# Optimization experiments

Measured on AMD Instinct MI355X. Metric: run time of the kernel, lower is better.

The kernel has to match this reference:

```python
import jax, jax.numpy as jnp
import numpy as np

D = 256      # d_model
NH = 8       # heads
HD = D // NH # head dim = 32
NL = 4       # feature levels
NP = 4       # sampling points per head per level
DFF = 1024   # ffn hidden
LAYERS = 6
SHAPES = [(48, 48), (24, 24), (12, 12), (6, 6)]


def setup_inputs() -> dict:
    key = jax.random.key(0)
    ks = jax.random.split(key, 20)
    bs = 2
    inp = {}
    for i, (h, w) in enumerate(SHAPES):
        inp[f"src{i}"] = jax.random.normal(ks[i], (bs, D, h, w), jnp.float32)
        inp[f"pos{i}"] = jax.random.normal(ks[4 + i], (bs, D, h, w), jnp.float32)

    def p(k, shape, s=0.02):
        return jax.random.normal(k, shape, jnp.float32) * s

    inp["level_embed"] = p(ks[8], (NL, D), 1.0)
    inp["Wv"] = p(ks[9], (LAYERS, D, D))
    inp["bv"] = jnp.zeros((LAYERS, D))
    inp["Woff"] = p(ks[10], (LAYERS, D, NH * NL * NP * 2), 0.001)
    inp["boff"] = p(ks[11], (LAYERS, NH * NL * NP * 2), 0.5)
    inp["Wa"] = p(ks[12], (LAYERS, D, NH * NL * NP))
    inp["ba"] = jnp.zeros((LAYERS, NH * NL * NP))
    inp["Wo"] = p(ks[13], (LAYERS, D, D))
    inp["bo"] = jnp.zeros((LAYERS, D))
    inp["g1"] = jnp.ones((LAYERS, D))
    inp["beta1"] = jnp.zeros((LAYERS, D))
    inp["W1"] = p(ks[14], (LAYERS, D, DFF))
    inp["bf1"] = jnp.zeros((LAYERS, DFF))
    inp["W2"] = p(ks[15], (LAYERS, DFF, D))
    inp["bf2"] = jnp.zeros((LAYERS, D))
    inp["g2"] = jnp.ones((LAYERS, D))
    inp["beta2"] = jnp.zeros((LAYERS, D))
    return inp


def _ln(x, g, b):
    m = x.mean(-1, keepdims=True)
    v = ((x - m) ** 2).mean(-1, keepdims=True)
    return (x - m) / jnp.sqrt(v + 1e-5) * g + b


def _bilinear(value, loc, H, W):
    # value: (bs, NH, H*W, HD); loc: (bs, Len, NH, NP, 2) in [0,1]
    # grid_sample, align_corners=False, zero padding
    bs, Len, nh, P, _ = loc.shape
    x = loc[..., 0] * W - 0.5
    y = loc[..., 1] * H - 0.5
    x0 = jnp.floor(x)
    y0 = jnp.floor(y)
    lx = x - x0
    ly = y - y0
    x0i = x0.astype(jnp.int32)
    y0i = y0.astype(jnp.int32)
    out = jnp.zeros((bs, nh, Len, P, value.shape[-1]), value.dtype)
    for dy, dx, w in ((0, 0, (1 - lx) * (1 - ly)), (0, 1, lx * (1 - ly)),
                      (1, 0, (1 - lx) * ly), (1, 1, lx * ly)):
        xi = x0i + dx
        yi = y0i + dy
        valid = (xi >= 0) & (xi < W) & (yi >= 0) & (yi < H)
        idx = jnp.clip(yi, 0, H - 1) * W + jnp.clip(xi, 0, W - 1)  # (bs,Len,NH,P)
        idx_t = idx.transpose(0, 2, 1, 3).reshape(bs, nh, Len * P)
        v = jnp.take_along_axis(value, idx_t[..., None], axis=2)
        v = v.reshape(bs, nh, Len, P, -1)
        wm = (w * valid).transpose(0, 2, 1, 3)  # (bs,NH,Len,P)
        out = out + v * wm[..., None]
    return out


def _msda(q, src, ref, shapes, starts, Wv, bv, Woff, boff, Wa, ba, Wo, bo):
    bs, Len, _ = q.shape
    value = (src @ Wv + bv).reshape(bs, Len, NH, HD)
    off = (q @ Woff + boff).reshape(bs, Len, NH, NL, NP, 2)
    attn = jax.nn.softmax((q @ Wa + ba).reshape(bs, Len, NH, NL * NP), -1)
    attn = attn.reshape(bs, Len, NH, NL, NP)
    acc = jnp.zeros((bs, NH, Len, HD), q.dtype)
    for lv, (H, W) in enumerate(shapes):
        norm = jnp.array([W, H], q.dtype)
        loc = ref[None, :, None, None, :] + off[:, :, :, lv] / norm  # (bs,Len,NH,NP,2)
        v = value[:, starts[lv]:starts[lv] + H * W].transpose(0, 2, 1, 3)
        samp = _bilinear(v, loc, H, W)  # (bs,NH,Len,NP,HD)
        acc = acc + (samp * attn[:, :, :, lv].transpose(0, 2, 1, 3)[..., None]).sum(3)
    return acc.transpose(0, 2, 1, 3).reshape(bs, Len, D) @ Wo + bo


def _encode(srcs, poss, level_embed, Wv, bv, Woff, boff, Wa, ba, Wo, bo,
            g1, beta1, W1, bf1, W2, bf2, g2, beta2):
    shapes = [(s.shape[2], s.shape[3]) for s in srcs]
    bs = srcs[0].shape[0]
    src_flat = jnp.concatenate(
        [s.reshape(bs, D, -1).transpose(0, 2, 1) for s in srcs], 1)
    pos_flat = jnp.concatenate(
        [p.reshape(bs, D, -1).transpose(0, 2, 1) + level_embed[i][None, None]
         for i, p in enumerate(poss)], 1)
    starts = np.cumsum([0] + [h * w for h, w in shapes])[:-1]
    # reference points (masks are all-zero so valid_ratios == 1)
    refs = []
    for (H, W) in shapes:
        ry, rx = jnp.meshgrid(jnp.linspace(0.5, H - 0.5, H) / H,
                              jnp.linspace(0.5, W - 0.5, W) / W, indexing='ij')
        refs.append(jnp.stack([rx.reshape(-1), ry.reshape(-1)], -1))
    ref = jnp.concatenate(refs, 0)  # (Len, 2)

    out = src_flat
    for l in range(LAYERS):
        q = out + pos_flat
        out2 = _msda(q, out, ref, shapes, starts, Wv[l], bv[l], Woff[l],
                     boff[l], Wa[l], ba[l], Wo[l], bo[l])
        out = _ln(out + out2, g1[l], beta1[l])
        h = jax.nn.relu(out @ W1[l] + bf1[l])
        out = _ln(out + h @ W2[l] + bf2[l], g2[l], beta2[l])
    return out, shapes, starts


def reference(src0, src1, src2, src3, pos0, pos1, pos2, pos3, level_embed,
              Wv, bv, Woff, boff, Wa, ba, Wo, bo,
              g1, beta1, W1, bf1, W2, bf2, g2, beta2):
    memory, shapes, starts = _encode(
        [src0, src1, src2, src3], [pos0, pos1, pos2, pos3], level_embed,
        Wv, bv, Woff, boff, Wa, ba, Wo, bo,
        g1, beta1, W1, bf1, W2, bf2, g2, beta2)
    spatial_shapes = jnp.array(shapes, jnp.int32)
    level_start_index = jnp.array(np.asarray(starts), jnp.int32)
    return memory, spatial_shapes, level_start_index
```

## Files before the change

kernel.cpp:

```cpp
#include <hip/hip_runtime.h>
#include <math.h>

#define D_MODEL 256
#define NHEAD 8
#define HDIM 32
#define NLVL 4
#define NPTS 4
#define DFF 1024
#define NLAYERS 6
#define LEN 3060
#define BS 2
#define MROWS (BS * LEN)
#define MPAD 6144

typedef __attribute__((ext_vector_type(8))) short bf16x8;
typedef __attribute__((ext_vector_type(4))) float f32x4;

__device__ __forceinline__ unsigned short f2bf(float f) {
    union { float f; unsigned u; } v; v.f = f;
    unsigned r = v.u + 0x7FFF + ((v.u >> 16) & 1);
    return (unsigned short)(r >> 16);
}

#define GLDS(gp, lp) __builtin_amdgcn_global_load_lds(                        \
    (const __attribute__((address_space(1))) void*)(gp),                      \
    (__attribute__((address_space(3))) void*)(lp), 16, 0, 0)

__global__ __launch_bounds__(256) void flatten_kernel(
    const float* __restrict__ s0, const float* __restrict__ s1,
    const float* __restrict__ s2, const float* __restrict__ s3,
    const float* __restrict__ p0, const float* __restrict__ p1,
    const float* __restrict__ p2, const float* __restrict__ p3,
    const float* __restrict__ lemb,
    float* __restrict__ out, unsigned short* __restrict__ outbf,
    float* __restrict__ pos)
{
    int gid = blockIdx.x * 256 + threadIdx.x;
    if (gid >= MROWS * D_MODEL) return;
    int d  = gid & (D_MODEL - 1);
    int bt = gid >> 8;
    int b  = (bt >= LEN) ? 1 : 0;
    int t  = bt - b * LEN;

    int lv, li, hw;
    const float* sp; const float* pp;
    if (t < 2304)      { lv = 0; li = t;        hw = 2304; sp = s0; pp = p0; }
    else if (t < 2880) { lv = 1; li = t - 2304; hw = 576;  sp = s1; pp = p1; }
    else if (t < 3024) { lv = 2; li = t - 2880; hw = 144;  sp = s2; pp = p2; }
    else               { lv = 3; li = t - 3024; hw = 36;   sp = s3; pp = p3; }

    size_t si = (size_t)(b * D_MODEL + d) * hw + li;
    float v = sp[si];
    out[gid]   = v;
    outbf[gid] = f2bf(v);
    pos[gid]   = pp[si] + lemb[lv * D_MODEL + d];
}

__global__ __launch_bounds__(256) void addq_kernel(
    const float4* __restrict__ a, const float4* __restrict__ b,
    ushort4* __restrict__ qbf, int n4)
{
    int i = blockIdx.x * 256 + threadIdx.x;
    if (i >= n4) return;
    float4 x = a[i], y = b[i];
    qbf[i] = make_ushort4(f2bf(x.x + y.x), f2bf(x.y + y.y),
                          f2bf(x.z + y.z), f2bf(x.w + y.w));
}

__global__ __launch_bounds__(256) void wconv_kernel(
    const float* __restrict__ Wv, const float* __restrict__ Woff,
    const float* __restrict__ Wa, const float* __restrict__ Wo,
    const float* __restrict__ W1, const float* __restrict__ W2,
    unsigned short* __restrict__ Wv_t, unsigned short* __restrict__ Woffa_t,
    unsigned short* __restrict__ Wo_t, unsigned short* __restrict__ W1_t,
    unsigned short* __restrict__ W2_t)
{
    __shared__ float tile[32][33];
    int bid = blockIdx.x;
    int layer = bid / 736, r = bid % 736;
    const float* src; unsigned short* dst;
    int N, tk, tn, dstRowOff = 0, dstLd;
    if (r < 64)       { src = Wv  + layer*65536;  dst = Wv_t   + layer*65536;  N = 256;  int t2 = r;       tk = t2 >> 3; tn = t2 & 7;  dstLd = 256;  }
    else if (r < 128) { src = Woff+ layer*65536;  dst = Woffa_t+ layer*98304;  N = 256;  int t2 = r - 64;  tk = t2 >> 3; tn = t2 & 7;  dstLd = 256;  }
    else if (r < 160) { src = Wa  + layer*32768;  dst = Woffa_t+ layer*98304;  N = 128;  int t2 = r - 128; tk = t2 >> 2; tn = t2 & 3;  dstLd = 256;  dstRowOff = 256; }
    else if (r < 224) { src = Wo  + layer*65536;  dst = Wo_t   + layer*65536;  N = 256;  int t2 = r - 160; tk = t2 >> 3; tn = t2 & 7;  dstLd = 256;  }
    else if (r < 480) { src = W1  + layer*262144; dst = W1_t   + layer*262144; N = 1024; int t2 = r - 224; tk = t2 >> 5; tn = t2 & 31; dstLd = 256;  }
    else              { src = W2  + layer*262144; dst = W2_t   + layer*262144; N = 256;  int t2 = r - 480; tk = t2 >> 3; tn = t2 & 7;  dstLd = 1024; }
    int k0 = tk * 32, n0 = tn * 32;
    int tx = threadIdx.x & 31, ty = threadIdx.x >> 5;
    #pragma unroll
    for (int i = 0; i < 4; ++i)
        tile[ty + i*8][tx] = src[(size_t)(k0 + ty + i*8) * N + n0 + tx];
    __syncthreads();
    #pragma unroll
    for (int i = 0; i < 4; ++i)
        dst[(size_t)(dstRowOff + n0 + ty + i*8) * dstLd + k0 + tx] =
            f2bf(tile[tx][ty + i*8]);
}

template<bool RELU, bool OUTBF>
__global__ __launch_bounds__(256) void mfma_gemm(
    const unsigned short* __restrict__ A, const unsigned short* __restrict__ Bt,
    const float* __restrict__ bias, const float* __restrict__ bias2, int split,
    void* __restrict__ Cout, int M, int N, int K)
{
    __shared__ __align__(16) unsigned short lds[6144];
    const int tid  = threadIdx.x;
    const int lane = tid & 63, wave = tid >> 6;
    const int wm = wave >> 1, wn = wave & 1;
    const int row0 = blockIdx.y * 128, col0 = blockIdx.x * 64;
    const int l15 = lane & 15, l4 = lane >> 4;
    char* ldsb = (char*)lds;

    const unsigned short* aSrc[2]; char* aDst[2];
    #pragma unroll
    for (int i = 0; i < 2; ++i) {
        int u = i*256 + wave*64 + lane;
        int rr = u >> 2, kb = u & 3, kbd = kb ^ (rr & 3);
        aSrc[i] = A + (size_t)(row0 + rr) * K + kbd * 8;
        aDst[i] = ldsb + (i*256 + wave*64) * 16;
    }
    const unsigned short* bSrc; char* bDst;
    {
        int u = tid, cc = u >> 2, kb = u & 3, kbd = kb ^ (cc & 3);
        bSrc = Bt + (size_t)(col0 + cc) * K + kbd * 8;
        bDst = ldsb + 8192 + wave * 1024;
    }

    int a_off[4], b_off[2];
    #pragma unroll
    for (int mf = 0; mf < 4; ++mf) {
        int rr = wm*64 + mf*16 + l15;
        a_off[mf] = rr*64 + ((l4 ^ (rr & 3)) << 4);
    }
    #pragma unroll
    for (int nf = 0; nf < 2; ++nf) {
        int cc = wn*32 + nf*16 + l15;
        b_off[nf] = 8192 + cc*64 + ((l4 ^ (cc & 3)) << 4);
    }

    f32x4 acc[4][2];
    #pragma unroll
    for (int mf = 0; mf < 4; ++mf)
        #pragma unroll
        for (int nf = 0; nf < 2; ++nf)
            acc[mf][nf] = (f32x4)(0.f);

    for (int k0 = 0; k0 < K; k0 += 32) {
        GLDS(aSrc[0] + k0, aDst[0]);
        GLDS(aSrc[1] + k0, aDst[1]);
        GLDS(bSrc    + k0, bDst);
        __syncthreads();
        bf16x8 bfr[2];
        #pragma unroll
        for (int nf = 0; nf < 2; ++nf)
            bfr[nf] = *(const bf16x8*)(ldsb + b_off[nf]);
        #pragma unroll
        for (int mf = 0; mf < 4; ++mf) {
            bf16x8 afr = *(const bf16x8*)(ldsb + a_off[mf]);
            #pragma unroll
            for (int nf = 0; nf < 2; ++nf)
                acc[mf][nf] = __builtin_amdgcn_mfma_f32_16x16x32_bf16(
                    afr, bfr[nf], acc[mf][nf], 0, 0, 0);
        }
        __syncthreads();
    }

    #pragma unroll
    for (int nf = 0; nf < 2; ++nf) {
        int col = col0 + wn*32 + nf*16 + l15;
        float bb = (col < split) ? bias[col] : bias2[col - split];
        #pragma unroll
        for (int mf = 0; mf < 4; ++mf) {
            #pragma unroll
            for (int i = 0; i < 4; ++i) {
                int row = row0 + wm*64 + mf*16 + l4*4 + i;
                if (row < M) {
                    float v = acc[mf][nf][i] + bb;
                    if (RELU) v = fmaxf(v, 0.f);
                    if (OUTBF)
                        ((unsigned short*)Cout)[(size_t)row * N + col] = f2bf(v);
                    else
                        ((float*)Cout)[(size_t)row * N + col] = v;
                }
            }
        }
    }
}

__global__ __launch_bounds__(256) void msda_kernel(
    const float* __restrict__ value,
    const float* __restrict__ offattn,
    unsigned short* __restrict__ outb)
{
    int gid = blockIdx.x * 256 + threadIdx.x;
    if (gid >= MROWS * NHEAD * 8) return;
    int part = gid & 7;
    int h    = (gid >> 3) & 7;
    int bt   = gid >> 6;
    int b    = (bt >= LEN) ? 1 : 0;
    int t    = bt - b * LEN;

    const float* lg = offattn + (size_t)bt * 384 + 256 + h * 16;
    float w[16];
    float mx = -1e30f;
    #pragma unroll
    for (int j = 0; j < 16; ++j) { w[j] = lg[j]; mx = fmaxf(mx, w[j]); }
    float s = 0.f;
    #pragma unroll
    for (int j = 0; j < 16; ++j) { w[j] = __expf(w[j] - mx); s += w[j]; }
    float inv = 1.f / s;

    int li, Wr;
    if (t < 2304)      { li = t;        Wr = 48; }
    else if (t < 2880) { li = t - 2304; Wr = 24; }
    else if (t < 3024) { li = t - 2880; Wr = 12; }
    else               { li = t - 3024; Wr = 6;  }
    float refx = ((li % Wr) + 0.5f) / (float)Wr;
    float refy = ((li / Wr) + 0.5f) / (float)Wr;

    const float* offp    = offattn + (size_t)bt * 384 + h * 32;
    const float* valbase = value + (size_t)b * LEN * D_MODEL + h * HDIM + part * 4;

    const int starts[4] = {0, 2304, 2880, 3024};
    const int Ws[4]     = {48, 24, 12, 6};

    float4 acc = make_float4(0.f, 0.f, 0.f, 0.f);

    #pragma unroll
    for (int lv = 0; lv < NLVL; ++lv) {
        int Wl = Ws[lv];
        int st = starts[lv];
        float fW = (float)Wl;
        #pragma unroll
        for (int p = 0; p < NPTS; ++p) {
            float ox = offp[(lv * NPTS + p) * 2 + 0];
            float oy = offp[(lv * NPTS + p) * 2 + 1];
            float x = (refx + ox / fW) * fW - 0.5f;
            float y = (refy + oy / fW) * fW - 0.5f;
            float x0f = floorf(x), y0f = floorf(y);
            float lx = x - x0f, ly = y - y0f;
            int x0 = (int)x0f, y0 = (int)y0f;
            float aw = w[lv * NPTS + p] * inv;
            float tw[4] = {(1.f - lx) * (1.f - ly), lx * (1.f - ly),
                           (1.f - lx) * ly,         lx * ly};
            const int dxs[4] = {0, 1, 0, 1};
            const int dys[4] = {0, 0, 1, 1};
            #pragma unroll
            for (int tap = 0; tap < 4; ++tap) {
                int xi = x0 + dxs[tap], yi = y0 + dys[tap];
                bool valid = (xi >= 0) & (xi < Wl) & (yi >= 0) & (yi < Wl);
                int xc = xi < 0 ? 0 : (xi > Wl - 1 ? Wl - 1 : xi);
                int yc = yi < 0 ? 0 : (yi > Wl - 1 ? Wl - 1 : yi);
                int tt = st + yc * Wl + xc;
                const float4 v = *(const float4*)(valbase + (size_t)tt * D_MODEL);
                float wt = valid ? aw * tw[tap] : 0.f;
                acc.x += wt * v.x; acc.y += wt * v.y;
                acc.z += wt * v.z; acc.w += wt * v.w;
            }
        }
    }
    ushort4 o = make_ushort4(f2bf(acc.x), f2bf(acc.y), f2bf(acc.z), f2bf(acc.w));
    *(ushort4*)(outb + (size_t)bt * D_MODEL + h * HDIM + part * 4) = o;
}

__global__ __launch_bounds__(256) void add_ln_kernel(
    float* __restrict__ out, unsigned short* __restrict__ outbf,
    const float* __restrict__ add,
    const float* __restrict__ g, const float* __restrict__ be)
{
    int row  = blockIdx.x * 4 + (threadIdx.x >> 6);
    int lane = threadIdx.x & 63;
    if (row >= MROWS) return;

    float4 x = ((const float4*)(out + (size_t)row * D_MODEL))[lane];
    float4 y = ((const float4*)(add + (size_t)row * D_MODEL))[lane];
    x.x += y.x; x.y += y.y; x.z += y.z; x.w += y.w;

    float s  = x.x + x.y + x.z + x.w;
    float ss = x.x * x.x + x.y * x.y + x.z * x.z + x.w * x.w;
    #pragma unroll
    for (int m = 1; m < 64; m <<= 1) {
        s  += __shfl_xor(s, m);
        ss += __shfl_xor(ss, m);
    }
    float mean = s * (1.f / 256.f);
    float var  = ss * (1.f / 256.f) - mean * mean;
    float rstd = rsqrtf(var + 1e-5f);

    float4 gv = ((const float4*)g)[lane];
    float4 bv = ((const float4*)be)[lane];
    float4 o;
    o.x = (x.x - mean) * rstd * gv.x + bv.x;
    o.y = (x.y - mean) * rstd * gv.y + bv.y;
    o.z = (x.z - mean) * rstd * gv.z + bv.z;
    o.w = (x.w - mean) * rstd * gv.w + bv.w;
    ((float4*)(out + (size_t)row * D_MODEL))[lane] = o;
    ((ushort4*)(outbf + (size_t)row * D_MODEL))[lane] =
        make_ushort4(f2bf(o.x), f2bf(o.y), f2bf(o.z), f2bf(o.w));
}

__global__ void tail_kernel(float* __restrict__ tail)
{
    if (threadIdx.x == 0 && blockIdx.x == 0) {
        const float vals[12] = {48.f, 48.f, 24.f, 24.f, 12.f, 12.f, 6.f, 6.f,
                                0.f, 2304.f, 2880.f, 3024.f};
        #pragma unroll
        for (int i = 0; i < 12; ++i) tail[i] = vals[i];
    }
}

extern "C" void kernel_launch(void* const* d_in, const int* in_sizes, int n_in,
                              void* d_out, int out_size, void* d_ws, size_t ws_size,
                              hipStream_t stream)
{
    const float* SRC[4]; const float* POS[4];
    bool interleaved = (in_sizes[1] == in_sizes[0]);
    if (interleaved) {
        SRC[0] = (const float*)d_in[0]; POS[0] = (const float*)d_in[1];
        SRC[1] = (const float*)d_in[2]; POS[1] = (const float*)d_in[3];
        SRC[2] = (const float*)d_in[4]; POS[2] = (const float*)d_in[5];
        SRC[3] = (const float*)d_in[6]; POS[3] = (const float*)d_in[7];
    } else {
        for (int i = 0; i < 4; ++i) {
            SRC[i] = (const float*)d_in[i];
            POS[i] = (const float*)d_in[4 + i];
        }
    }
    const float* lemb  = (const float*)d_in[8];
    const float* Wv    = (const float*)d_in[9];
    const float* bv    = (const float*)d_in[10];
    const float* Woff  = (const float*)d_in[11];
    const float* boff  = (const float*)d_in[12];
    const float* Wa    = (const float*)d_in[13];
    const float* ba    = (const float*)d_in[14];
    const float* Wo    = (const float*)d_in[15];
    const float* bo    = (const float*)d_in[16];
    const float* g1    = (const float*)d_in[17];
    const float* beta1 = (const float*)d_in[18];
    const float* W1    = (const float*)d_in[19];
    const float* bf1   = (const float*)d_in[20];
    const float* W2    = (const float*)d_in[21];
    const float* bf2   = (const float*)d_in[22];
    const float* g2    = (const float*)d_in[23];
    const float* beta2 = (const float*)d_in[24];

    float* out = (float*)d_out;

    char* ws = (char*)d_ws;
    float* pos     = (float*)ws;                                   ws += (size_t)MPAD * 256 * 4;
    float* val     = (float*)ws;                                   ws += (size_t)MPAD * 256 * 4;
    float* offattn = (float*)ws;                                   ws += (size_t)MPAD * 384 * 4;
    float* tmp     = (float*)ws;                                   ws += (size_t)MPAD * 256 * 4;
    unsigned short* qbf    = (unsigned short*)ws;                  ws += (size_t)MPAD * 256 * 2;
    unsigned short* outbf  = (unsigned short*)ws;                  ws += (size_t)MPAD * 256 * 2;
    unsigned short* msdabf = (unsigned short*)ws;                  ws += (size_t)MPAD * 256 * 2;
    unsigned short* hbuf   = (unsigned short*)ws;                  ws += (size_t)MPAD * 1024 * 2;
    unsigned short* Wv_t    = (unsigned short*)ws;                 ws += (size_t)6 * 65536 * 2;
    unsigned short* Woffa_t = (unsigned short*)ws;                 ws += (size_t)6 * 98304 * 2;
    unsigned short* Wo_t    = (unsigned short*)ws;                 ws += (size_t)6 * 65536 * 2;
    unsigned short* W1_t    = (unsigned short*)ws;                 ws += (size_t)6 * 262144 * 2;
    unsigned short* W2_t    = (unsigned short*)ws;                 ws += (size_t)6 * 262144 * 2;

    wconv_kernel<<<6 * 736, 256, 0, stream>>>(Wv, Woff, Wa, Wo, W1, W2,
                                              Wv_t, Woffa_t, Wo_t, W1_t, W2_t);

    const int nElem = MROWS * D_MODEL;
    flatten_kernel<<<(nElem + 255) / 256, 256, 0, stream>>>(
        SRC[0], SRC[1], SRC[2], SRC[3], POS[0], POS[1], POS[2], POS[3],
        lemb, out, outbf, pos);

    const int n4 = nElem / 4;
    const dim3 g256(256 / 64, MPAD / 128);
    const dim3 g384(384 / 64, MPAD / 128);
    const dim3 g1024(1024 / 64, MPAD / 128);

    for (int l = 0; l < NLAYERS; ++l) {
        const unsigned short* Wv_l   = Wv_t    + (size_t)l * 65536;
        const unsigned short* Woffa_l= Woffa_t + (size_t)l * 98304;
        const unsigned short* Wo_l   = Wo_t    + (size_t)l * 65536;
        const unsigned short* W1_l   = W1_t    + (size_t)l * 262144;
        const unsigned short* W2_l   = W2_t    + (size_t)l * 262144;
        const float* bv_l  = bv   + l * 256;
        const float* boff_l= boff + l * 256;
        const float* ba_l  = ba   + l * 128;
        const float* bo_l  = bo   + l * 256;
        const float* bf1_l = bf1  + l * DFF;
        const float* bf2_l = bf2  + l * 256;

        addq_kernel<<<(n4 + 255) / 256, 256, 0, stream>>>(
            (const float4*)out, (const float4*)pos, (ushort4*)qbf, n4);

        mfma_gemm<false, false><<<g256, 256, 0, stream>>>(
            outbf, Wv_l, bv_l, bv_l, 256, val, MROWS, 256, 256);

        mfma_gemm<false, false><<<g384, 256, 0, stream>>>(
            qbf, Woffa_l, boff_l, ba_l, 256, offattn, MROWS, 384, 256);

        msda_kernel<<<(MROWS * NHEAD * 8 + 255) / 256, 256, 0, stream>>>(
            val, offattn, msdabf);

        mfma_gemm<false, false><<<g256, 256, 0, stream>>>(
            msdabf, Wo_l, bo_l, bo_l, 256, tmp, MROWS, 256, 256);

        add_ln_kernel<<<MROWS / 4, 256, 0, stream>>>(
            out, outbf, tmp, g1 + l * 256, beta1 + l * 256);

        mfma_gemm<true, true><<<g1024, 256, 0, stream>>>(
            outbf, W1_l, bf1_l, bf1_l, 1024, hbuf, MROWS, 1024, 256);

        mfma_gemm<false, false><<<g256, 256, 0, stream>>>(
            hbuf, W2_l, bf2_l, bf2_l, 256, tmp, MROWS, 256, 1024);

        add_ln_kernel<<<MROWS / 4, 256, 0, stream>>>(
            out, outbf, tmp, g2 + l * 256, beta2 + l * 256);
    }

    tail_kernel<<<1, 64, 0, stream>>>(out + (size_t)MROWS * D_MODEL);
}
```

Measured before the change: 744.0 us.

## Fuse GEMM with residual LayerNorm, double-buffer GEMM tiles, store value in bf16

```diff
diff --git a/kernel.cpp b/kernel.cpp
--- a/kernel.cpp
+++ b/kernel.cpp
@@ -21,6 +21,10 @@
     unsigned r = v.u + 0x7FFF + ((v.u >> 16) & 1);
     return (unsigned short)(r >> 16);
 }
+__device__ __forceinline__ float bf2f(unsigned short s) {
+    union { unsigned u; float f; } v; v.u = ((unsigned)s) << 16;
+    return v.f;
+}
 
 #define GLDS(gp, lp) __builtin_amdgcn_global_load_lds(                        \
     (const __attribute__((address_space(1))) void*)(gp),                      \
@@ -33,7 +37,7 @@
     const float* __restrict__ p2, const float* __restrict__ p3,
     const float* __restrict__ lemb,
     float* __restrict__ out, unsigned short* __restrict__ outbf,
-    float* __restrict__ pos)
+    unsigned short* __restrict__ qbf, float* __restrict__ pos)
 {
     int gid = blockIdx.x * 256 + threadIdx.x;
     if (gid >= MROWS * D_MODEL) return;
@@ -51,20 +55,11 @@
 
     size_t si = (size_t)(b * D_MODEL + d) * hw + li;
     float v = sp[si];
+    float pv = pp[si] + lemb[lv * D_MODEL + d];
     out[gid]   = v;
     outbf[gid] = f2bf(v);
-    pos[gid]   = pp[si] + lemb[lv * D_MODEL + d];
-}
-
-__global__ __launch_bounds__(256) void addq_kernel(
-    const float4* __restrict__ a, const float4* __restrict__ b,
-    ushort4* __restrict__ qbf, int n4)
-{
-    int i = blockIdx.x * 256 + threadIdx.x;
-    if (i >= n4) return;
-    float4 x = a[i], y = b[i];
-    qbf[i] = make_ushort4(f2bf(x.x + y.x), f2bf(x.y + y.y),
-                          f2bf(x.z + y.z), f2bf(x.w + y.w));
+    qbf[gid]   = f2bf(v + pv);
+    pos[gid]   = pv;
 }
 
 __global__ __launch_bounds__(256) void wconv_kernel(
@@ -99,82 +94,64 @@
 }
 
 template<bool RELU, bool OUTBF>
-__global__ __launch_bounds__(256) void mfma_gemm(
+__global__ __launch_bounds__(256) void gemm2(
     const unsigned short* __restrict__ A, const unsigned short* __restrict__ Bt,
     const float* __restrict__ bias, const float* __restrict__ bias2, int split,
     void* __restrict__ Cout, int M, int N, int K)
 {
-    __shared__ __align__(16) unsigned short lds[6144];
+    __shared__ __align__(16) char smem[16384];
     const int tid  = threadIdx.x;
     const int lane = tid & 63, wave = tid >> 6;
     const int wm = wave >> 1, wn = wave & 1;
-    const int row0 = blockIdx.y * 128, col0 = blockIdx.x * 64;
+    const int row0 = blockIdx.y * 64, col0 = blockIdx.x * 64;
     const int l15 = lane & 15, l4 = lane >> 4;
-    char* ldsb = (char*)lds;
-
-    const unsigned short* aSrc[2]; char* aDst[2];
-    #pragma unroll
-    for (int i = 0; i < 2; ++i) {
-        int u = i*256 + wave*64 + lane;
-        int rr = u >> 2, kb = u & 3, kbd = kb ^ (rr & 3);
-        aSrc[i] = A + (size_t)(row0 + rr) * K + kbd * 8;
-        aDst[i] = ldsb + (i*256 + wave*64) * 16;
-    }
-    const unsigned short* bSrc; char* bDst;
-    {
-        int u = tid, cc = u >> 2, kb = u & 3, kbd = kb ^ (cc & 3);
-        bSrc = Bt + (size_t)(col0 + cc) * K + kbd * 8;
-        bDst = ldsb + 8192 + wave * 1024;
-    }
-
-    int a_off[4], b_off[2];
-    #pragma unroll
-    for (int mf = 0; mf < 4; ++mf) {
-        int rr = wm*64 + mf*16 + l15;
-        a_off[mf] = rr*64 + ((l4 ^ (rr & 3)) << 4);
-    }
-    #pragma unroll
-    for (int nf = 0; nf < 2; ++nf) {
-        int cc = wn*32 + nf*16 + l15;
-        b_off[nf] = 8192 + cc*64 + ((l4 ^ (cc & 3)) << 4);
-    }
-
-    f32x4 acc[4][2];
-    #pragma unroll
-    for (int mf = 0; mf < 4; ++mf)
-        #pragma unroll
-        for (int nf = 0; nf < 2; ++nf)
-            acc[mf][nf] = (f32x4)(0.f);
-
-    for (int k0 = 0; k0 < K; k0 += 32) {
-        GLDS(aSrc[0] + k0, aDst[0]);
-        GLDS(aSrc[1] + k0, aDst[1]);
-        GLDS(bSrc    + k0, bDst);
-        __syncthreads();
-        bf16x8 bfr[2];
-        #pragma unroll
-        for (int nf = 0; nf < 2; ++nf)
-            bfr[nf] = *(const bf16x8*)(ldsb + b_off[nf]);
-        #pragma unroll
-        for (int mf = 0; mf < 4; ++mf) {
-            bf16x8 afr = *(const bf16x8*)(ldsb + a_off[mf]);
+
+    const int kb = tid >> 6, ix = tid & 63;
+    const unsigned short* aSrc = A  + (size_t)(row0 + ix) * K + kb * 8;
+    const unsigned short* bSrc = Bt + (size_t)(col0 + ix) * K + kb * 8;
+    char* aDst = smem + wave * 1024;
+    char* bDst = smem + 4096 + wave * 1024;
+
+    const int aOff0 = ((l4 * 64 + wm * 32 + l15) << 4);
+    const int bOff0 = 4096 + ((l4 * 64 + wn * 32 + l15) << 4);
+
+    f32x4 acc[2][2] = {};
+
+    GLDS(aSrc, aDst);
+    GLDS(bSrc, bDst);
+    __syncthreads();
+
+    const int nk = K >> 5;
+    for (int t = 0; t < nk; ++t) {
+        const int bo = (t & 1) * 8192;
+        if (t + 1 < nk) {
+            const int nbo = ((t + 1) & 1) * 8192;
+            GLDS(aSrc + ((t + 1) << 5), aDst + nbo);
+            GLDS(bSrc + ((t + 1) << 5), bDst + nbo);
+        }
+        bf16x8 av[2], bv[2];
+        av[0] = *(const bf16x8*)(smem + bo + aOff0);
+        av[1] = *(const bf16x8*)(smem + bo + aOff0 + 256);
+        bv[0] = *(const bf16x8*)(smem + bo + bOff0);
+        bv[1] = *(const bf16x8*)(smem + bo + bOff0 + 256);
+        #pragma unroll
+        for (int mf = 0; mf < 2; ++mf)
             #pragma unroll
             for (int nf = 0; nf < 2; ++nf)
                 acc[mf][nf] = __builtin_amdgcn_mfma_f32_16x16x32_bf16(
-                    afr, bfr[nf], acc[mf][nf], 0, 0, 0);
-        }
+                    av[mf], bv[nf], acc[mf][nf], 0, 0, 0);
         __syncthreads();
     }
 
     #pragma unroll
     for (int nf = 0; nf < 2; ++nf) {
-        int col = col0 + wn*32 + nf*16 + l15;
+        int col = col0 + wn * 32 + nf * 16 + l15;
         float bb = (col < split) ? bias[col] : bias2[col - split];
         #pragma unroll
-        for (int mf = 0; mf < 4; ++mf) {
+        for (int mf = 0; mf < 2; ++mf) {
             #pragma unroll
             for (int i = 0; i < 4; ++i) {
-                int row = row0 + wm*64 + mf*16 + l4*4 + i;
+                int row = row0 + wm * 32 + mf * 16 + l4 * 4 + i;
                 if (row < M) {
                     float v = acc[mf][nf][i] + bb;
                     if (RELU) v = fmaxf(v, 0.f);
@@ -188,8 +165,136 @@
     }
 }
 
+template<bool WITH_POS>
+__global__ __launch_bounds__(512) void gemm_ln(
+    const unsigned short* __restrict__ A, const unsigned short* __restrict__ Bt,
+    const float* __restrict__ bias, const float* __restrict__ g,
+    const float* __restrict__ be, const float* __restrict__ pos,
+    float* __restrict__ out, unsigned short* __restrict__ outbf,
+    unsigned short* __restrict__ qbf, int K)
+{
+    __shared__ __align__(16) char smem[38912];
+    float* st = (float*)(smem + 36864);
+    const int tid  = threadIdx.x;
+    const int lane = tid & 63, wave = tid >> 6;
+    const int l15 = lane & 15, l4 = lane >> 4;
+    const int row0 = blockIdx.x * 32;
+
+    const unsigned short* aSrc = nullptr;
+    char* aDst = nullptr;
+    if (tid < 128) {
+        int kb = tid >> 5, rr = tid & 31;
+        aSrc = A + (size_t)(row0 + rr) * K + kb * 8;
+        aDst = smem + wave * 1024;
+    }
+    const unsigned short* bSrc0;
+    const unsigned short* bSrc1;
+    {
+        int u0 = tid,        kb0 = u0 >> 8, c0 = u0 & 255;
+        int u1 = 512 + tid,  kb1 = u1 >> 8, c1 = u1 & 255;
+        bSrc0 = Bt + (size_t)c0 * K + kb0 * 8;
+        bSrc1 = Bt + (size_t)c1 * K + kb1 * 8;
+    }
+    char* bDst0 = smem + 4096 + (wave * 64) * 16;
+    char* bDst1 = smem + 4096 + (512 + wave * 64) * 16;
+
+    const int aOff0 = ((l4 * 32 + l15) << 4);
+    const int bOff0 = 4096 + ((l4 * 256 + wave * 32 + l15) << 4);
+
+    f32x4 acc[2][2] = {};
+
+    if (aSrc) GLDS(aSrc, aDst);
+    GLDS(bSrc0, bDst0);
+    GLDS(bSrc1, bDst1);
+    __syncthreads();
+
+    const int nk = K >> 5;
+    for (int t = 0; t < nk; ++t) {
+        const int abo = (t & 1) * 2048, bbo = (t & 1) * 16384;
+        if (t + 1 < nk) {
+            const int nabo = ((t + 1) & 1) * 2048, nbbo = ((t + 1) & 1) * 16384;
+            if (aSrc) GLDS(aSrc + ((t + 1) << 5), aDst + nabo);
+            GLDS(bSrc0 + ((t + 1) << 5), bDst0 + nbbo);
+            GLDS(bSrc1 + ((t + 1) << 5), bDst1 + nbbo);
+        }
+        bf16x8 av[2], bv[2];
+        av[0] = *(const bf16x8*)(smem + abo + aOff0);
+        av[1] = *(const bf16x8*)(smem + abo + aOff0 + 256);
+        bv[0] = *(const bf16x8*)(smem + bbo + bOff0);
+        bv[1] = *(const bf16x8*)(smem + bbo + bOff0 + 256);
+        #pragma unroll
+        for (int mf = 0; mf < 2; ++mf)
+            #pragma unroll
+            for (int nf = 0; nf < 2; ++nf)
+                acc[mf][nf] = __builtin_amdgcn_mfma_f32_16x16x32_bf16(
+                    av[mf], bv[nf], acc[mf][nf], 0, 0, 0);
+        __syncthreads();
+    }
+
+    #pragma unroll
+    for (int mf = 0; mf < 2; ++mf)
+        #pragma unroll
+        for (int i = 0; i < 4; ++i) {
+            int row = row0 + mf * 16 + l4 * 4 + i;
+            bool ok = row < MROWS;
+            #pragma unroll
+            for (int nf = 0; nf < 2; ++nf) {
+                int col = wave * 32 + nf * 16 + l15;
+                float r = ok ? out[(size_t)row * 256 + col] : 0.f;
+                acc[mf][nf][i] += bias[col] + r;
+            }
+        }
+
+    #pragma unroll
+    for (int mf = 0; mf < 2; ++mf)
+        #pragma unroll
+        for (int i = 0; i < 4; ++i) {
+            float s  = acc[mf][0][i] + acc[mf][1][i];
+            float ss = acc[mf][0][i] * acc[mf][0][i]
+                     + acc[mf][1][i] * acc[mf][1][i];
+            #pragma unroll
+            for (int m = 1; m < 16; m <<= 1) {
+                s  += __shfl_xor(s, m);
+                ss += __shfl_xor(ss, m);
+            }
+            if (l15 == 0) {
+                int r = mf * 16 + l4 * 4 + i;
+                st[wave * 32 + r]       = s;
+                st[256 + wave * 32 + r] = ss;
+            }
+        }
+    __syncthreads();
+
+    #pragma unroll
+    for (int mf = 0; mf < 2; ++mf)
+        #pragma unroll
+        for (int i = 0; i < 4; ++i) {
+            int r = mf * 16 + l4 * 4 + i;
+            float s = 0.f, ss = 0.f;
+            #pragma unroll
+            for (int w = 0; w < 8; ++w) {
+                s  += st[w * 32 + r];
+                ss += st[256 + w * 32 + r];
+            }
+            float mean = s * (1.f / 256.f);
+            float var  = ss * (1.f / 256.f) - mean * mean;
+            float rstd = rsqrtf(var + 1e-5f);
+            int row = row0 + r;
+            if (row >= MROWS) continue;
+            #pragma unroll
+            for (int nf = 0; nf < 2; ++nf) {
+                int col = wave * 32 + nf * 16 + l15;
+                float o = (acc[mf][nf][i] - mean) * rstd * g[col] + be[col];
+                size_t idx = (size_t)row * 256 + col;
+                out[idx]   = o;
+                outbf[idx] = f2bf(o);
+                if (WITH_POS) qbf[idx] = f2bf(o + pos[idx]);
+            }
+        }
+}
+
 __global__ __launch_bounds__(256) void msda_kernel(
-    const float* __restrict__ value,
+    const unsigned short* __restrict__ value,
     const float* __restrict__ offattn,
     unsigned short* __restrict__ outb)
 {
@@ -219,8 +324,9 @@
     float refx = ((li % Wr) + 0.5f) / (float)Wr;
     float refy = ((li / Wr) + 0.5f) / (float)Wr;
 
-    const float* offp    = offattn + (size_t)bt * 384 + h * 32;
-    const float* valbase = value + (size_t)b * LEN * D_MODEL + h * HDIM + part * 4;
+    const float* offp = offattn + (size_t)bt * 384 + h * 32;
+    const unsigned short* valbase =
+        value + (size_t)b * LEN * D_MODEL + h * HDIM + part * 4;
 
     const int starts[4] = {0, 2304, 2880, 3024};
     const int Ws[4]     = {48, 24, 12, 6};
@@ -230,7 +336,7 @@
     #pragma unroll
     for (int lv = 0; lv < NLVL; ++lv) {
         int Wl = Ws[lv];
-        int st = starts[lv];
+        int stt = starts[lv];
         float fW = (float)Wl;
         #pragma unroll
         for (int p = 0; p < NPTS; ++p) {
@@ -252,52 +358,16 @@
                 bool valid = (xi >= 0) & (xi < Wl) & (yi >= 0) & (yi < Wl);
                 int xc = xi < 0 ? 0 : (xi > Wl - 1 ? Wl - 1 : xi);
                 int yc = yi < 0 ? 0 : (yi > Wl - 1 ? Wl - 1 : yi);
-                int tt = st + yc * Wl + xc;
-                const float4 v = *(const float4*)(valbase + (size_t)tt * D_MODEL);
+                int tt = stt + yc * Wl + xc;
+                ushort4 vv = *(const ushort4*)(valbase + (size_t)tt * D_MODEL);
                 float wt = valid ? aw * tw[tap] : 0.f;
-                acc.x += wt * v.x; acc.y += wt * v.y;
-                acc.z += wt * v.z; acc.w += wt * v.w;
+                acc.x += wt * bf2f(vv.x); acc.y += wt * bf2f(vv.y);
+                acc.z += wt * bf2f(vv.z); acc.w += wt * bf2f(vv.w);
             }
         }
     }
     ushort4 o = make_ushort4(f2bf(acc.x), f2bf(acc.y), f2bf(acc.z), f2bf(acc.w));
     *(ushort4*)(outb + (size_t)bt * D_MODEL + h * HDIM + part * 4) = o;
-}
-
-__global__ __launch_bounds__(256) void add_ln_kernel(
-    float* __restrict__ out, unsigned short* __restrict__ outbf,
-    const float* __restrict__ add,
-    const float* __restrict__ g, const float* __restrict__ be)
-{
-    int row  = blockIdx.x * 4 + (threadIdx.x >> 6);
-    int lane = threadIdx.x & 63;
-    if (row >= MROWS) return;
-
-    float4 x = ((const float4*)(out + (size_t)row * D_MODEL))[lane];
-    float4 y = ((const float4*)(add + (size_t)row * D_MODEL))[lane];
-    x.x += y.x; x.y += y.y; x.z += y.z; x.w += y.w;
-
-    float s  = x.x + x.y + x.z + x.w;
-    float ss = x.x * x.x + x.y * x.y + x.z * x.z + x.w * x.w;
-    #pragma unroll
-    for (int m = 1; m < 64; m <<= 1) {
-        s  += __shfl_xor(s, m);
-        ss += __shfl_xor(ss, m);
-    }
-    float mean = s * (1.f / 256.f);
-    float var  = ss * (1.f / 256.f) - mean * mean;
-    float rstd = rsqrtf(var + 1e-5f);
-
-    float4 gv = ((const float4*)g)[lane];
-    float4 bv = ((const float4*)be)[lane];
-    float4 o;
-    o.x = (x.x - mean) * rstd * gv.x + bv.x;
-    o.y = (x.y - mean) * rstd * gv.y + bv.y;
-    o.z = (x.z - mean) * rstd * gv.z + bv.z;
-    o.w = (x.w - mean) * rstd * gv.w + bv.w;
-    ((float4*)(out + (size_t)row * D_MODEL))[lane] = o;
-    ((ushort4*)(outbf + (size_t)row * D_MODEL))[lane] =
-        make_ushort4(f2bf(o.x), f2bf(o.y), f2bf(o.z), f2bf(o.w));
 }
 
 __global__ void tail_kernel(float* __restrict__ tail)
@@ -348,19 +418,18 @@
     float* out = (float*)d_out;
 
     char* ws = (char*)d_ws;
-    float* pos     = (float*)ws;                                   ws += (size_t)MPAD * 256 * 4;
-    float* val     = (float*)ws;                                   ws += (size_t)MPAD * 256 * 4;
-    float* offattn = (float*)ws;                                   ws += (size_t)MPAD * 384 * 4;
-    float* tmp     = (float*)ws;                                   ws += (size_t)MPAD * 256 * 4;
-    unsigned short* qbf    = (unsigned short*)ws;                  ws += (size_t)MPAD * 256 * 2;
-    unsigned short* outbf  = (unsigned short*)ws;                  ws += (size_t)MPAD * 256 * 2;
-    unsigned short* msdabf = (unsigned short*)ws;                  ws += (size_t)MPAD * 256 * 2;
-    unsigned short* hbuf   = (unsigned short*)ws;                  ws += (size_t)MPAD * 1024 * 2;
-    unsigned short* Wv_t    = (unsigned short*)ws;                 ws += (size_t)6 * 65536 * 2;
-    unsigned short* Woffa_t = (unsigned short*)ws;                 ws += (size_t)6 * 98304 * 2;
-    unsigned short* Wo_t    = (unsigned short*)ws;                 ws += (size_t)6 * 65536 * 2;
-    unsigned short* W1_t    = (unsigned short*)ws;                 ws += (size_t)6 * 262144 * 2;
-    unsigned short* W2_t    = (unsigned short*)ws;                 ws += (size_t)6 * 262144 * 2;
+    float* pos     = (float*)ws;                   ws += (size_t)MPAD * 256 * 4;
+    float* offattn = (float*)ws;                   ws += (size_t)MPAD * 384 * 4;
+    unsigned short* qbf    = (unsigned short*)ws;  ws += (size_t)MPAD * 256 * 2;
+    unsigned short* outbf  = (unsigned short*)ws;  ws += (size_t)MPAD * 256 * 2;
+    unsigned short* msdabf = (unsigned short*)ws;  ws += (size_t)MPAD * 256 * 2;
+    unsigned short* valbf  = (unsigned short*)ws;  ws += (size_t)MPAD * 256 * 2;
+    unsigned short* hbuf   = (unsigned short*)ws;  ws += (size_t)MPAD * 1024 * 2;
+    unsigned short* Wv_t    = (unsigned short*)ws; ws += (size_t)6 * 65536 * 2;
+    unsigned short* Woffa_t = (unsigned short*)ws; ws += (size_t)6 * 98304 * 2;
+    unsigned short* Wo_t    = (unsigned short*)ws; ws += (size_t)6 * 65536 * 2;
+    unsigned short* W1_t    = (unsigned short*)ws; ws += (size_t)6 * 262144 * 2;
+    unsigned short* W2_t    = (unsigned short*)ws; ws += (size_t)6 * 262144 * 2;
 
     wconv_kernel<<<6 * 736, 256, 0, stream>>>(Wv, Woff, Wa, Wo, W1, W2,
                                               Wv_t, Woffa_t, Wo_t, W1_t, W2_t);
@@ -368,52 +437,39 @@
     const int nElem = MROWS * D_MODEL;
     flatten_kernel<<<(nElem + 255) / 256, 256, 0, stream>>>(
         SRC[0], SRC[1], SRC[2], SRC[3], POS[0], POS[1], POS[2], POS[3],
-        lemb, out, outbf, pos);
-
-    const int n4 = nElem / 4;
-    const dim3 g256(256 / 64, MPAD / 128);
-    const dim3 g384(384 / 64, MPAD / 128);
-    const dim3 g1024(1024 / 64, MPAD / 128);
+        lemb, out, outbf, qbf, pos);
+
+    const dim3 g256(4, MPAD / 64);
+    const dim3 g384(6, MPAD / 64);
+    const dim3 g1024(16, MPAD / 64);
+    const int gLN = MPAD / 32;
 
     for (int l = 0; l < NLAYERS; ++l) {
-        const unsigned short* Wv_l   = Wv_t    + (size_t)l * 65536;
-        const unsigned short* Woffa_l= Woffa_t + (size_t)l * 98304;
-        const unsigned short* Wo_l   = Wo_t    + (size_t)l * 65536;
-        const unsigned short* W1_l   = W1_t    + (size_t)l * 262144;
-        const unsigned short* W2_l   = W2_t    + (size_t)l * 262144;
-        const float* bv_l  = bv   + l * 256;
-        const float* boff_l= boff + l * 256;
-        const float* ba_l  = ba   + l * 128;
-        const float* bo_l  = bo   + l * 256;
-        const float* bf1_l = bf1  + l * DFF;
-        const float* bf2_l = bf2  + l * 256;
-
-        addq_kernel<<<(n4 + 255) / 256, 256, 0, stream>>>(
-            (const float4*)out, (const float4*)pos, (ushort4*)qbf, n4);
-
-        mfma_gemm<false, false><<<g256, 256, 0, stream>>>(
-            outbf, Wv_l, bv_l, bv_l, 256, val, MROWS, 256, 256);
-
-        mfma_gemm<false, false><<<g384, 256, 0, stream>>>(
-            qbf, Woffa_l, boff_l, ba_l, 256, offattn, MROWS, 384, 256);
+        const unsigned short* Wv_l    = Wv_t    + (size_t)l * 65536;
+        const unsigned short* Woffa_l = Woffa_t + (size_t)l * 98304;
+        const unsigned short* Wo_l    = Wo_t    + (size_t)l * 65536;
+        const unsigned short* W1_l    = W1_t    + (size_t)l * 262144;
+        const unsigned short* W2_l    = W2_t    + (size_t)l * 262144;
+
+        gemm2<false, true><<<g256, 256, 0, stream>>>(
+            outbf, Wv_l, bv + l * 256, bv + l * 256, 256, valbf, MROWS, 256, 256);
+
+        gemm2<false, false><<<g384, 256, 0, stream>>>(
+            qbf, Woffa_l, boff + l * 256, ba + l * 128, 256, offattn, MROWS, 384, 256);
 
         msda_kernel<<<(MROWS * NHEAD * 8 + 255) / 256, 256, 0, stream>>>(
-            val, offattn, msdabf);
-
-        mfma_gemm<false, false><<<g256, 256, 0, stream>>>(
-            msdabf, Wo_l, bo_l, bo_l, 256, tmp, MROWS, 256, 256);
-
-        add_ln_kernel<<<MROWS / 4, 256, 0, stream>>>(
-            out, outbf, tmp, g1 + l * 256, beta1 + l * 256);
-
-        mfma_gemm<true, true><<<g1024, 256, 0, stream>>>(
-            outbf, W1_l, bf1_l, bf1_l, 1024, hbuf, MROWS, 1024, 256);
-
-        mfma_gemm<false, false><<<g256, 256, 0, stream>>>(
-            hbuf, W2_l, bf2_l, bf2_l, 256, tmp, MROWS, 256, 1024);
-
-        add_ln_kernel<<<MROWS / 4, 256, 0, stream>>>(
-            out, outbf, tmp, g2 + l * 256, beta2 + l * 256);
+            valbf, offattn, msdabf);
+
+        gemm_ln<false><<<gLN, 512, 0, stream>>>(
+            msdabf, Wo_l, bo + l * 256, g1 + l * 256, beta1 + l * 256, pos,
+            out, outbf, qbf, 256);
+
+        gemm2<true, true><<<g1024, 256, 0, stream>>>(
+            outbf, W1_l, bf1 + l * DFF, bf1 + l * DFF, 1024, hbuf, MROWS, 1024, 256);
+
+        gemm_ln<true><<<gLN, 512, 0, stream>>>(
+            hbuf, W2_l, bf2 + l * 256, g2 + l * 256, beta2 + l * 256, pos,
+            out, outbf, qbf, 1024);
     }
 
     tail_kernel<<<1, 64, 0, stream>>>(out + (size_t)MROWS * D_MODEL);
```

Result: slower. 770.9 us (+3.6%).
